# Kernel optimization log

Measured on AMD Instinct MI355X. Metric: run time of the kernel, lower is better.

Reference implementation:

```python
import jax, jax.numpy as jnp
import numpy as np

B, C_IN, N = 64, 1, 8192
WIDTH, MODES, NLAYERS = 64, 16, 4


def setup_inputs() -> dict:
    key = jax.random.key(0)
    ks = jax.random.split(key, 10)
    scale = 1.0 / (WIDTH * WIDTH)
    inp = {
        "x": jax.random.normal(ks[0], (B, C_IN, N), dtype=jnp.float32),
        # lifting p: Linear(2, width)
        "p_w": jax.random.normal(ks[1], (WIDTH, 2), dtype=jnp.float32) * 0.5,
        "p_b": jax.random.normal(ks[2], (WIDTH,), dtype=jnp.float32) * 0.1,
        # 4 spectral conv weights, complex stored as real/imag (uniform like torch.rand cfloat)
        "sc_wr": scale * jax.random.uniform(ks[3], (NLAYERS, WIDTH, WIDTH, MODES), dtype=jnp.float32),
        "sc_wi": scale * jax.random.uniform(ks[4], (NLAYERS, WIDTH, WIDTH, MODES), dtype=jnp.float32),
        # 4 pointwise (1x1) conv weights/biases
        "w_w": jax.random.normal(ks[5], (NLAYERS, WIDTH, WIDTH), dtype=jnp.float32) / np.sqrt(WIDTH),
        "w_b": jax.random.normal(ks[6], (NLAYERS, WIDTH), dtype=jnp.float32) * 0.1,
        # projection q: Linear(width, 1)
        "q_w": jax.random.normal(ks[7], (1, WIDTH), dtype=jnp.float32) / np.sqrt(WIDTH),
        "q_b": jax.random.normal(ks[8], (1,), dtype=jnp.float32) * 0.1,
    }
    return inp


def spectral_conv(x, wr, wi, n):
    # x: [b, i, n] real; weights complex [i, o, modes]
    x_ft = jnp.fft.rfft(x, axis=-1)                      # [b, i, n//2+1] complex
    w = (wr + 1j * wi).astype(jnp.complex64)
    out_modes = jnp.einsum('bix,iox->box', x_ft[:, :, :MODES], w)
    out_ft = jnp.zeros((x.shape[0], w.shape[1], n // 2 + 1), dtype=jnp.complex64)
    out_ft = out_ft.at[:, :, :MODES].set(out_modes)
    return jnp.fft.irfft(out_ft, n=n, axis=-1)


def reference(x, p_w, p_b, sc_wr, sc_wi, w_w, w_b, q_w, q_b):
    b, _, n = x.shape
    grid = jnp.broadcast_to(jnp.linspace(0.0, 1.0, n, dtype=jnp.float32)[None, None, :], (b, 1, n))
    h = jnp.concatenate([x, grid], axis=1)               # [b, 2, n]
    # lifting: Linear over channel dim
    h = jnp.einsum('bcn,wc->bwn', h, p_w) + p_b[None, :, None]
    for l in range(NLAYERS):
        x1 = spectral_conv(h, sc_wr[l], sc_wi[l], n)
        x2 = jnp.einsum('bin,oi->bon', h, w_w[l]) + w_b[l][None, :, None]
        h = jax.nn.gelu(x1 + x2, approximate=False)
    out = jnp.einsum('bwn,ow->bon', h, q_w) + q_b[None, :, None]  # [b, 1, n]
    return out
```

## Files before the change

kernel.cpp:

```cpp
#include <hip/hip_runtime.h>
#include <math.h>


typedef _Float16 f16;
typedef _Float16 f16x2 __attribute__((ext_vector_type(2)));
typedef _Float16 f16x4 __attribute__((ext_vector_type(4)));
typedef _Float16 f16x8 __attribute__((ext_vector_type(8)));
typedef float    f32x2 __attribute__((ext_vector_type(2)));
typedef float    f32x4 __attribute__((ext_vector_type(4)));
typedef unsigned int u32;

#define BB 64
#define NN 8192

#define HT_S 64
#define HO_S 136
#define WS_S 72
#define MS_S 40
#define BI_S 40
#define BF_S 136

__device__ __forceinline__ int ht_swz(int n) { return ((n & 7) ^ ((n >> 3) & 7)) << 3; }

__device__ __forceinline__ float gelu_f(float v) {
    float x  = v * 0.70710678118654752f;
    float ax = fabsf(x);
    float t  = __builtin_amdgcn_rcpf(fmaf(0.3275911f, ax, 1.0f));
    float p  = fmaf(1.061405429f, t, -1.453152027f);
    p = fmaf(p, t, 1.421413741f);
    p = fmaf(p, t, -0.284496736f);
    p = fmaf(p, t, 0.254829592f);
    p = p * t;
    float e  = __expf(-x * x);
    float er = fmaf(-p, e, 1.0f);
    er = copysignf(er, x);
    return 0.5f * fmaf(v, er, v);
}

__global__ __launch_bounds__(256) void fill_basis(f16* __restrict__ basF,
                                                  f16* __restrict__ basI,
                                                  const float* __restrict__ w_w,
                                                  f16* __restrict__ Wh,
                                                  float* __restrict__ Sz) {
    int n = blockIdx.x * 256 + threadIdx.x;
    f16 row[32];
#pragma unroll
    for (int k = 0; k < 16; ++k) {
        float s, c;
        sincospif((float)(k * n) * (1.0f / 4096.0f), &s, &c);
        basF[k * NN + n]        = (f16)c;
        basF[(16 + k) * NN + n] = (f16)(-s);
        row[2 * k]     = (f16)c;
        row[2 * k + 1] = (f16)s;
    }
#pragma unroll
    for (int q = 0; q < 4; ++q) *(f16x8*)&basI[n * 32 + 8 * q] = *(f16x8*)&row[8 * q];
    Wh[n]        = (f16)w_w[n];
    Wh[n + 8192] = (f16)w_w[n + 8192];
    f32x4* S4 = (f32x4*)Sz;
    f32x4 z = {0.f, 0.f, 0.f, 0.f};
#pragma unroll
    for (int u = 0; u < 4; ++u) S4[n * 4 + u] = z;
}

__global__ __launch_bounds__(1024) void mode_mix(float* __restrict__ S,
                                                 const float* __restrict__ wr,
                                                 const float* __restrict__ wi,
                                                 f16* __restrict__ Mph) {
    int b = blockIdx.x, t = threadIdx.x;
    __shared__ float Ss[32 * 66];
    if (t < 512) {
        f32x4 v = *(const f32x4*)&S[b * 2048 + t * 4];
        int rw = t >> 4, cl = (t & 15) * 4;
#pragma unroll
        for (int e = 0; e < 4; ++e) Ss[rw * 66 + cl + e] = v[e];
    }
    __syncthreads();
    *(f32x2*)&S[b * 2048 + t * 2] = (f32x2){0.f, 0.f};

    int o = t >> 4, k = t & 15;
    const float* wrp = wr + o * 16 + k;
    const float* wip = wi + o * 16 + k;
    float ar = 0.f, ai = 0.f;
#pragma unroll 8
    for (int i = 0; i < 64; ++i) {
        float sr = Ss[k * 66 + i], si = Ss[(16 + k) * 66 + i];
        float wrv = wrp[i * 1024];
        float wiv = wip[i * 1024];
        ar = fmaf(sr, wrv, ar); ar = fmaf(-si, wiv, ar);
        ai = fmaf(sr, wiv, ai); ai = fmaf(si, wrv, ai);
    }
    float sc = (k == 0 ? 1.0f : 2.0f) * (1.0f / 8192.0f);
    f16x2 outv = { (f16)(sc * ar), (f16)(-sc * ai) };
    *(f16x2*)&Mph[b * 2048 + o * 32 + 2 * k] = outv;
}

__device__ __forceinline__ void dft_accum(const f16* Hout, const f16* BasF,
                                          f32x4 sacc[2], int lane, int wv) {
    int q = lane >> 4, l15 = lane & 15;
    int o = (wv << 4) + l15;
#pragma unroll
    for (int ks = 0; ks < 4; ++ks) {
        f16x8 bh = *(const f16x8*)&Hout[o * HO_S + ks * 32 + q * 8];
#pragma unroll
        for (int mt = 0; mt < 2; ++mt) {
            f16x8 af = *(const f16x8*)&BasF[(mt * 16 + l15) * BF_S + ks * 32 + q * 8];
            sacc[mt] = __builtin_amdgcn_mfma_f32_16x16x32_f16(af, bh, sacc[mt], 0, 0, 0);
        }
    }
}

__device__ __forceinline__ void dft_flush(const f32x4 sacc[2], float* __restrict__ S,
                                          int b, int lane, int wv) {
    int q = lane >> 4, l15 = lane & 15;
#pragma unroll
    for (int mt = 0; mt < 2; ++mt)
#pragma unroll
        for (int r = 0; r < 4; ++r)
            atomicAdd(&S[(b * 32 + mt * 16 + q * 4 + r) * 64 + (wv << 4) + l15],
                      sacc[mt][r]);
}

__global__ __launch_bounds__(256, 3) void lift_kernel(const float* __restrict__ x,
                                                      const float* __restrict__ p_w,
                                                      const float* __restrict__ p_b,
                                                      f16* __restrict__ h,
                                                      const f16* __restrict__ basF_g,
                                                      float* __restrict__ S) {
    __shared__ f16 Hout[64 * HO_S];
    __shared__ f16 BasF[32 * BF_S];
    int t = threadIdx.x;
    int b = blockIdx.x >> 5;
    int g = blockIdx.x & 31;
    int lane = t & 63, wv = t >> 6;

    float w0[4], w1[4], pb[4];
#pragma unroll
    for (int r = 0; r < 4; ++r) {
        int o = (t >> 4) + 16 * r;
        w0[r] = p_w[2 * o]; w1[r] = p_w[2 * o + 1]; pb[r] = p_b[o];
    }

    f32x4 sacc[2] = {{0.f,0.f,0.f,0.f},{0.f,0.f,0.f,0.f}};
#pragma unroll
    for (int tile = 0; tile < 2; ++tile) {
        int n0 = ((g << 1) + tile) << 7;
#pragma unroll
        for (int r = 0; r < 4; ++r) {
            int o = (t >> 4) + 16 * r;
            int ns = (t & 15) << 3;
            f16 vals[8];
#pragma unroll
            for (int j = 0; j < 8; ++j) {
                int n = n0 + ns + j;
                float xv = x[(b << 13) + n];
                vals[j] = (f16)(w0[r] * xv + w1[r] * ((float)n * (1.0f / 8191.0f)) + pb[r]);
            }
            *(f16x8*)&Hout[o * HO_S + ns] = *(f16x8*)vals;
            *(f16x8*)(h + (((size_t)(b * 64 + o)) << 13) + n0 + ns) = *(f16x8*)vals;
        }
#pragma unroll
        for (int u = 0; u < 2; ++u) {
            int km = t >> 3, nn = (t & 7) * 16 + u * 8;
            *(f16x8*)&BasF[km * BF_S + nn] = *(const f16x8*)&basF_g[km * NN + n0 + nn];
        }
        __syncthreads();
        dft_accum(Hout, BasF, sacc, lane, wv);
        if (tile == 0) __syncthreads();
    }
    dft_flush(sacc, S, b, lane, wv);
}

template <int DO_DFT>
__global__ __launch_bounds__(256, 3) void layer_kernel(f16* __restrict__ h,
                                                       const f16* __restrict__ Wl_h,
                                                       const float* __restrict__ bl,
                                                       const f16* __restrict__ Mph,
                                                       const f16* __restrict__ basF_g,
                                                       const f16* __restrict__ basI_g,
                                                       float* __restrict__ S,
                                                       const float* __restrict__ q_w,
                                                       const float* __restrict__ q_b,
                                                       float* __restrict__ out) {
    constexpr int TILES = DO_DFT ? 2 : 1;
    constexpr int GPB   = 64 / TILES;
    __shared__ __align__(16) char pool[16384 + 9216];
    f16* Ht   = (f16*)pool;
    f16* Ws   = (f16*)(pool + 16384);
    f16* Hout = (f16*)pool;
    __shared__ f16 Ms2[64 * MS_S];
    __shared__ f16 BasI[128 * BI_S];
    __shared__ f16 BasF[32 * BF_S];
    __shared__ float bls[64];
    int t = threadIdx.x;
    int b = blockIdx.x / GPB;
    int g = blockIdx.x % GPB;
    f16* hbase = h + (((size_t)(b * 64)) << 13);
    int lane = t & 63, wv = t >> 6;
    int q = lane >> 4, l15 = lane & 15;

    if (t >= 128) {
        int t2 = t - 128;
        {
            int o = t2 & 63, hs = (t2 >> 6) * 32;
            const f16* src = Wl_h + o * 64 + hs;
            f16* dst = &Ws[o * WS_S + hs];
#pragma unroll
            for (int u = 0; u < 4; ++u) *(f16x8*)&dst[8 * u] = *(const f16x8*)&src[8 * u];
        }
        {
            int o = t2 >> 1, seg = (t2 & 1) * 16;
            const f16* src = Mph + b * 2048 + o * 32 + seg;
            f16* dst = &Ms2[o * MS_S + seg];
            *(f16x8*)&dst[0] = *(const f16x8*)&src[0];
            *(f16x8*)&dst[8] = *(const f16x8*)&src[8];
        }
    }
    if (t < 64) bls[t] = bl[t];

    f16x8 Bw[4][2], Bm[4];
    f32x4 sacc[2] = {{0.f,0.f,0.f,0.f},{0.f,0.f,0.f,0.f}};

    for (int tile = 0; tile < TILES; ++tile) {
        int n0 = (g * TILES + tile) << 7;
        f16* hbt = hbase + n0;

        if (t < 128) {
            int ig = t >> 4, nb = t & 15;
            int i0 = ig << 3, ns = nb << 3;
            f16x8 R[8];
#pragma unroll
            for (int k = 0; k < 8; ++k)
                R[k] = *(const f16x8*)(hbt + ((size_t)(i0 + k) << 13) + ns);
            const u32* rd = (const u32*)R;
            int swz = nb & 7;
#pragma unroll
            for (int j = 0; j < 8; ++j) {
                u32 o[4] __attribute__((aligned(16)));
                u32 sel = (j & 1) ? 0x07060302u : 0x05040100u;
                int jd = j >> 1;
#pragma unroll
                for (int e = 0; e < 4; ++e)
                    o[e] = __builtin_amdgcn_perm(rd[(2 * e + 1) * 4 + jd],
                                                 rd[(2 * e) * 4 + jd], sel);
                int col = i0 ^ ((j ^ swz) << 3);
                *(f16x8*)&Ht[(ns + j) * HT_S + col] = *(const f16x8*)o;
            }
        } else {
            int t2 = t - 128;
            {
                const f16* src = basI_g + (size_t)(n0 + t2) * 32;
                f16* dst = &BasI[t2 * BI_S];
#pragma unroll
                for (int u = 0; u < 4; ++u) *(f16x8*)&dst[8 * u] = *(const f16x8*)&src[8 * u];
            }
            if (DO_DFT) {
                int km = t2 >> 2, seg = (t2 & 3) * 32;
                const f16* src = basF_g + km * NN + n0 + seg;
                f16* dst = &BasF[km * BF_S + seg];
#pragma unroll
                for (int u = 0; u < 4; ++u) *(f16x8*)&dst[8 * u] = *(const f16x8*)&src[8 * u];
            }
        }
        __syncthreads();

        if (tile == 0) {
#pragma unroll
            for (int ct = 0; ct < 4; ++ct) {
#pragma unroll
                for (int ks = 0; ks < 2; ++ks)
                    Bw[ct][ks] = *(const f16x8*)&Ws[(ct * 16 + l15) * WS_S + ks * 32 + q * 8];
                Bm[ct] = *(const f16x8*)&Ms2[(ct * 16 + l15) * MS_S + q * 8];
            }
        }

        f32x4 acc[4][2];
#pragma unroll
        for (int ct = 0; ct < 4; ++ct)
#pragma unroll
            for (int m = 0; m < 2; ++m) acc[ct][m] = (f32x4){0.f, 0.f, 0.f, 0.f};

#pragma unroll
        for (int mtl = 0; mtl < 2; ++mtl) {
            int nrow = (2 * wv + mtl) * 16 + l15;
            const f16* hrow = &Ht[nrow * HT_S];
            int g3 = ht_swz(nrow);
#pragma unroll
            for (int ks = 0; ks < 2; ++ks) {
                f16x8 Ah = *(const f16x8*)&hrow[(ks * 32 + q * 8) ^ g3];
#pragma unroll
                for (int ct = 0; ct < 4; ++ct)
                    acc[ct][mtl] = __builtin_amdgcn_mfma_f32_16x16x32_f16(
                        Ah, Bw[ct][ks], acc[ct][mtl], 0, 0, 0);
            }
            f16x8 Ab = *(const f16x8*)&BasI[nrow * BI_S + q * 8];
#pragma unroll
            for (int ct = 0; ct < 4; ++ct)
                acc[ct][mtl] = __builtin_amdgcn_mfma_f32_16x16x32_f16(
                    Ab, Bm[ct], acc[ct][mtl], 0, 0, 0);
        }

        float bv[4];
#pragma unroll
        for (int ct = 0; ct < 4; ++ct) bv[ct] = bls[ct * 16 + l15];
        __syncthreads();
#pragma unroll
        for (int ct = 0; ct < 4; ++ct) {
            int o = ct * 16 + l15;
#pragma unroll
            for (int mtl = 0; mtl < 2; ++mtl) {
                int nbase = (2 * wv + mtl) * 16 + q * 4;
                float gg[4];
#pragma unroll
                for (int r = 0; r < 4; ++r)
                    gg[r] = gelu_f(acc[ct][mtl][r] + bv[ct]);
                f16x2 lo = __builtin_bit_cast(f16x2, __builtin_amdgcn_cvt_pkrtz(gg[0], gg[1]));
                f16x2 hi = __builtin_bit_cast(f16x2, __builtin_amdgcn_cvt_pkrtz(gg[2], gg[3]));
                f16x4 pk = {lo[0], lo[1], hi[0], hi[1]};
                *(f16x4*)&Hout[o * HO_S + nbase] = pk;
            }
        }
        __syncthreads();

        if (DO_DFT) {
            dft_accum(Hout, BasF, sacc, lane, wv);
#pragma unroll
            for (int r = 0; r < 4; ++r) {
                int o = (t >> 4) + 16 * r;
                int ns = (t & 15) << 3;
                *(f16x8*)(hbt + ((size_t)o << 13) + ns) = *(f16x8*)&Hout[o * HO_S + ns];
            }
        } else {
            if (t < 128) {
                int n = t;
                float s = q_b[0];
#pragma unroll 8
                for (int o = 0; o < 64; ++o) s += q_w[o] * (float)Hout[o * HO_S + n];
                out[(b << 13) + n0 + n] = s;
            }
        }
        if (tile != TILES - 1) __syncthreads();
    }
    if (DO_DFT) dft_flush(sacc, S, b, lane, wv);
}

extern "C" void kernel_launch(void* const* d_in, const int* in_sizes, int n_in,
                              void* d_out, int out_size, void* d_ws, size_t ws_size,
                              hipStream_t stream) {
    const float* x     = (const float*)d_in[0];
    const float* p_w   = (const float*)d_in[1];
    const float* p_b   = (const float*)d_in[2];
    const float* sc_wr = (const float*)d_in[3];
    const float* sc_wi = (const float*)d_in[4];
    const float* w_w   = (const float*)d_in[5];
    const float* w_b   = (const float*)d_in[6];
    const float* q_w   = (const float*)d_in[7];
    const float* q_b   = (const float*)d_in[8];
    float* out = (float*)d_out;

    char* ws = (char*)d_ws;
    f16*   h    = (f16*)ws;
    float* S    = (float*)(ws + 67108864ull);
    f16*   Mph  = (f16*)(ws + 67633152ull);
    f16*   basF = (f16*)(ws + 67895296ull);
    f16*   basI = (f16*)(ws + 68419584ull);
    f16*   Wh   = (f16*)(ws + 68943872ull);

    hipLaunchKernelGGL(fill_basis, dim3(NN / 256), dim3(256), 0, stream,
                       basF, basI, w_w, Wh, S);
    hipLaunchKernelGGL(lift_kernel, dim3(BB * 32), dim3(256), 0, stream,
                       x, p_w, p_b, h, basF, S);
    for (int l = 0; l < 4; ++l) {
        hipLaunchKernelGGL(mode_mix, dim3(BB), dim3(1024), 0, stream,
                           S, sc_wr + l * 65536, sc_wi + l * 65536, Mph);
        if (l < 3) {
            hipLaunchKernelGGL((layer_kernel<1>), dim3(BB * 32), dim3(256), 0, stream,
                               h, Wh + l * 4096, w_b + l * 64, Mph, basF, basI, S,
                               q_w, q_b, out);
        } else {
            hipLaunchKernelGGL((layer_kernel<0>), dim3(BB * 64), dim3(256), 0, stream,
                               h, Wh + l * 4096, w_b + l * 64, Mph, basF, basI, S,
                               q_w, q_b, out);
        }
    }
}
```

Measured before the change: 262.7 us.

## Prefetch h tiles up front, fuse projection into registers, vectorize lift loads

The layer kernel now issues the global loads for both 128-column h tiles at kernel start, so they overlap with the weight and mode staging instead of being issued per tile. The final layer now handles two tiles per block like the others and computes the q projection straight from the accumulator registers, using a 16-lane shuffle reduction. This removes the Hout staging and its two barriers. The lift kernel loads x as float4 vectors once per tile instead of scalar loads repeated for each of the four output rows. The cost is more live registers (16 f16x8 per thread), which could reduce occupancy or cause spills under the 3-blocks launch bound.

```diff
diff --git a/kernel.cpp b/kernel.cpp
--- a/kernel.cpp
+++ b/kernel.cpp
@@ -133,6 +133,7 @@
     int b = blockIdx.x >> 5;
     int g = blockIdx.x & 31;
     int lane = t & 63, wv = t >> 6;
+    int ns = (t & 15) << 3;
 
     float w0[4], w1[4], pb[4];
 #pragma unroll
@@ -141,19 +142,26 @@
         w0[r] = p_w[2 * o]; w1[r] = p_w[2 * o + 1]; pb[r] = p_b[o];
     }
 
-    f32x4 sacc[2] = {{0.f,0.f,0.f,0.f},{0.f,0.f,0.f,0.f}};
+    f32x4 X[2][2];
 #pragma unroll
     for (int tile = 0; tile < 2; ++tile) {
         int n0 = ((g << 1) + tile) << 7;
+        X[tile][0] = *(const f32x4*)&x[(b << 13) + n0 + ns];
+        X[tile][1] = *(const f32x4*)&x[(b << 13) + n0 + ns + 4];
+    }
+
+    f32x4 sacc[2] = {{0.f,0.f,0.f,0.f},{0.f,0.f,0.f,0.f}};
+#pragma unroll
+    for (int tile = 0; tile < 2; ++tile) {
+        int n0 = ((g << 1) + tile) << 7;
 #pragma unroll
         for (int r = 0; r < 4; ++r) {
             int o = (t >> 4) + 16 * r;
-            int ns = (t & 15) << 3;
             f16 vals[8];
 #pragma unroll
             for (int j = 0; j < 8; ++j) {
                 int n = n0 + ns + j;
-                float xv = x[(b << 13) + n];
+                float xv = X[tile][j >> 2][j & 3];
                 vals[j] = (f16)(w0[r] * xv + w1[r] * ((float)n * (1.0f / 8191.0f)) + pb[r]);
             }
             *(f16x8*)&Hout[o * HO_S + ns] = *(f16x8*)vals;
@@ -182,8 +190,7 @@
                                                        const float* __restrict__ q_w,
                                                        const float* __restrict__ q_b,
                                                        float* __restrict__ out) {
-    constexpr int TILES = DO_DFT ? 2 : 1;
-    constexpr int GPB   = 64 / TILES;
+    constexpr int TILES = 2;
     __shared__ __align__(16) char pool[16384 + 9216];
     f16* Ht   = (f16*)pool;
     f16* Ws   = (f16*)(pool + 16384);
@@ -193,13 +200,26 @@
     __shared__ f16 BasF[32 * BF_S];
     __shared__ float bls[64];
     int t = threadIdx.x;
-    int b = blockIdx.x / GPB;
-    int g = blockIdx.x % GPB;
+    int b = blockIdx.x >> 5;
+    int g = blockIdx.x & 31;
     f16* hbase = h + (((size_t)(b * 64)) << 13);
     int lane = t & 63, wv = t >> 6;
     int q = lane >> 4, l15 = lane & 15;
 
-    if (t >= 128) {
+    f16x8 R[2][8];
+    int i0 = 0, nb = 0;
+    if (t < 128) {
+        int ig = t >> 4; nb = t & 15;
+        i0 = ig << 3;
+        int ns = nb << 3;
+#pragma unroll
+        for (int tile = 0; tile < TILES; ++tile) {
+            const f16* hbt = hbase + ((g * TILES + tile) << 7);
+#pragma unroll
+            for (int k = 0; k < 8; ++k)
+                R[tile][k] = *(const f16x8*)(hbt + ((size_t)(i0 + k) << 13) + ns);
+        }
+    } else {
         int t2 = t - 128;
         {
             int o = t2 & 63, hs = (t2 >> 6) * 32;
@@ -226,13 +246,8 @@
         f16* hbt = hbase + n0;
 
         if (t < 128) {
-            int ig = t >> 4, nb = t & 15;
-            int i0 = ig << 3, ns = nb << 3;
-            f16x8 R[8];
-#pragma unroll
-            for (int k = 0; k < 8; ++k)
-                R[k] = *(const f16x8*)(hbt + ((size_t)(i0 + k) << 13) + ns);
-            const u32* rd = (const u32*)R;
+            int ns = nb << 3;
+            const u32* rd = (const u32*)R[tile];
             int swz = nb & 7;
 #pragma unroll
             for (int j = 0; j < 8; ++j) {
@@ -303,41 +318,58 @@
         float bv[4];
 #pragma unroll
         for (int ct = 0; ct < 4; ++ct) bv[ct] = bls[ct * 16 + l15];
-        __syncthreads();
-#pragma unroll
-        for (int ct = 0; ct < 4; ++ct) {
-            int o = ct * 16 + l15;
-#pragma unroll
-            for (int mtl = 0; mtl < 2; ++mtl) {
-                int nbase = (2 * wv + mtl) * 16 + q * 4;
-                float gg[4];
-#pragma unroll
-                for (int r = 0; r < 4; ++r)
-                    gg[r] = gelu_f(acc[ct][mtl][r] + bv[ct]);
-                f16x2 lo = __builtin_bit_cast(f16x2, __builtin_amdgcn_cvt_pkrtz(gg[0], gg[1]));
-                f16x2 hi = __builtin_bit_cast(f16x2, __builtin_amdgcn_cvt_pkrtz(gg[2], gg[3]));
-                f16x4 pk = {lo[0], lo[1], hi[0], hi[1]};
-                *(f16x4*)&Hout[o * HO_S + nbase] = pk;
-            }
-        }
-        __syncthreads();
 
         if (DO_DFT) {
+            __syncthreads();
+#pragma unroll
+            for (int ct = 0; ct < 4; ++ct) {
+                int o = ct * 16 + l15;
+#pragma unroll
+                for (int mtl = 0; mtl < 2; ++mtl) {
+                    int nbase = (2 * wv + mtl) * 16 + q * 4;
+                    float gg[4];
+#pragma unroll
+                    for (int r = 0; r < 4; ++r)
+                        gg[r] = gelu_f(acc[ct][mtl][r] + bv[ct]);
+                    f16x2 lo = __builtin_bit_cast(f16x2, __builtin_amdgcn_cvt_pkrtz(gg[0], gg[1]));
+                    f16x2 hi = __builtin_bit_cast(f16x2, __builtin_amdgcn_cvt_pkrtz(gg[2], gg[3]));
+                    f16x4 pk = {lo[0], lo[1], hi[0], hi[1]};
+                    *(f16x4*)&Hout[o * HO_S + nbase] = pk;
+                }
+            }
+            __syncthreads();
             dft_accum(Hout, BasF, sacc, lane, wv);
 #pragma unroll
             for (int r = 0; r < 4; ++r) {
                 int o = (t >> 4) + 16 * r;
-                int ns = (t & 15) << 3;
-                *(f16x8*)(hbt + ((size_t)o << 13) + ns) = *(f16x8*)&Hout[o * HO_S + ns];
+                int ns2 = (t & 15) << 3;
+                *(f16x8*)(hbt + ((size_t)o << 13) + ns2) = *(f16x8*)&Hout[o * HO_S + ns2];
             }
         } else {
-            if (t < 128) {
-                int n = t;
-                float s = q_b[0];
-#pragma unroll 8
-                for (int o = 0; o < 64; ++o) s += q_w[o] * (float)Hout[o * HO_S + n];
-                out[(b << 13) + n0 + n] = s;
-            }
+            float qv[4];
+#pragma unroll
+            for (int ct = 0; ct < 4; ++ct) qv[ct] = q_w[ct * 16 + l15];
+            float part[2][4] = {{0.f,0.f,0.f,0.f},{0.f,0.f,0.f,0.f}};
+#pragma unroll
+            for (int ct = 0; ct < 4; ++ct)
+#pragma unroll
+                for (int mtl = 0; mtl < 2; ++mtl)
+#pragma unroll
+                    for (int r = 0; r < 4; ++r)
+                        part[mtl][r] = fmaf(qv[ct],
+                            gelu_f(acc[ct][mtl][r] + bv[ct]), part[mtl][r]);
+#pragma unroll
+            for (int mtl = 0; mtl < 2; ++mtl)
+#pragma unroll
+                for (int r = 0; r < 4; ++r) {
+                    float s = part[mtl][r];
+#pragma unroll
+                    for (int m = 1; m < 16; m <<= 1)
+                        s += __shfl_xor(s, m, 64);
+                    if (l15 == 0)
+                        out[(b << 13) + n0 + (2 * wv + mtl) * 16 + q * 4 + r] =
+                            s + q_b[0];
+                }
         }
         if (tile != TILES - 1) __syncthreads();
     }
@@ -378,7 +410,7 @@
                                h, Wh + l * 4096, w_b + l * 64, Mph, basF, basI, S,
                                q_w, q_b, out);
         } else {
-            hipLaunchKernelGGL((layer_kernel<0>), dim3(BB * 64), dim3(256), 0, stream,
+            hipLaunchKernelGGL((layer_kernel<0>), dim3(BB * 32), dim3(256), 0, stream,
                                h, Wh + l * 4096, w_b + l * 64, Mph, basF, basI, S,
                                q_w, q_b, out);
         }
```

After: 263.0 us. Within noise of the previous version (+0.1%).
